# Kernel tuning notes

Measured on AMD Instinct MI355X. Metric: run time of the kernel, lower is better.

The kernel has to match this reference:

```python
import jax, jax.numpy as jnp
import numpy as np

B, K, NQ = 16, 4, 10  # batch, n_blocks, n_qubits
DIM = 2 ** NQ


def setup_inputs() -> dict:
    key = jax.random.key(0)
    k1, k2 = jax.random.split(key)
    weights = jax.random.normal(k1, (B, K, 1, NQ, 1, 1), dtype=jnp.float32)
    state = jax.random.normal(k2, (B, K, 1, DIM, 1), dtype=jnp.float32)
    return {"weights": weights, "state": state}


def _rx_mats(weights):
    # weights: (B, K, 1, NQ, 1, 1) real angles -> per-qubit Rx 2x2: [[cos, -i sin], [-i sin, cos]]
    w = weights[..., 0, 0]  # (B, K, 1, NQ)
    a = jnp.cos(w / 2).astype(jnp.complex64)
    b = jnp.sin(w / 2).astype(jnp.complex64)
    eye = jnp.eye(2, dtype=jnp.complex64)
    offx = jnp.array([[0.0, 1.0], [1.0, 0.0]], dtype=jnp.complex64)
    return a[..., None, None] * eye - 1j * b[..., None, None] * offx  # (B,K,1,NQ,2,2)


def _kron_chain(rxs):
    # rxs: (B, K, 1, NQ, 2, 2) -> U: (B, K, 1, 2**NQ, 2**NQ)
    U = rxs[..., 0, :, :]
    for q in range(1, rxs.shape[-3]):
        m = U.shape[-1]
        Rq = rxs[..., q, :, :]
        # kron(U, Rq): outer product over matrix indices, then merge
        U = (U[..., :, None, :, None] * Rq[..., None, :, None, :]).reshape(*U.shape[:-2], 2 * m, 2 * m)
    return U


def reference(weights, state):
    U = _kron_chain(_rx_mats(weights))              # (B,K,1,2^n,2^n) complex64
    psi = state.astype(jnp.complex64)               # (B,K,1,2^n,1)
    return jnp.matmul(U, psi)                       # (B,K,1,2^n,1) complex64
```

## Files before the change

### kernel.cpp

```cpp
#include <hip/hip_runtime.h>

constexpr int BK  = 16 * 4;
constexpr int NQ  = 10;
constexpr int DIM = 1 << NQ;

__global__ __launch_bounds__(512)
void rx_layer_kernel(const float* __restrict__ weights,
                     const float* __restrict__ state,
                     float* __restrict__ out_re,
                     float* __restrict__ out_im)
{
    __shared__ float re[DIM];
    __shared__ float im[DIM];

    const int bk = blockIdx.x;
    const int t  = threadIdx.x;

    const float* st = state + bk * DIM;
    re[t]       = st[t];       im[t]       = 0.0f;
    re[t + 512] = st[t + 512]; im[t + 512] = 0.0f;

    const float* w = weights + bk * NQ;

    #pragma unroll
    for (int q = 0; q < NQ; ++q) {
        __syncthreads();
        const float wv = w[q];
        const float a  = cosf(0.5f * wv);
        const float b  = sinf(0.5f * wv);

        const int s  = 1 << (NQ - 1 - q);
        const int i0 = ((t & ~(s - 1)) << 1) | (t & (s - 1));
        const int i1 = i0 + s;

        const float x0r = re[i0], x0i = im[i0];
        const float x1r = re[i1], x1i = im[i1];

        re[i0] = a * x0r + b * x1i;
        im[i0] = a * x0i - b * x1r;
        re[i1] = a * x1r + b * x0i;
        im[i1] = a * x1i - b * x0r;
    }
    __syncthreads();

    float* orr = out_re + bk * DIM;
    orr[t]       = re[t];
    orr[t + 512] = re[t + 512];
    if (out_im != nullptr) {
        float* oi = out_im + bk * DIM;
        oi[t]       = im[t];
        oi[t + 512] = im[t + 512];
    }
}

extern "C" void kernel_launch(void* const* d_in, const int* in_sizes, int n_in,
                              void* d_out, int out_size, void* d_ws, size_t ws_size,
                              hipStream_t stream) {
    const float* weights = (const float*)d_in[0];
    const float* state   = (const float*)d_in[1];
    float* out = (float*)d_out;

    float* out_re = out;
    float* out_im = nullptr;
    if (out_size >= 2 * BK * DIM) {
        out_im = out + BK * DIM;
    }
    rx_layer_kernel<<<BK, 512, 0, stream>>>(weights, state, out_re, out_im);
}
```

Baseline: 57.57 us.

## Apply Rx gates in registers with one wavefront per block using lane shuffles

Replaces the 512-thread shared-memory kernel, which needed a barrier per qubit, with a single 64-lane wavefront per state vector that holds 16 amplitudes per lane in registers. High qubits are applied through cross-lane shuffles and low qubits through in-register butterflies. The first gate uses the fact that the input is real to skip the imaginary work. It drops all LDS traffic and __syncthreads, and vectorises global loads and stores with float4. The trade-off is far fewer threads in flight (64 blocks of 64 threads) and an unconditional write of the imaginary output.

Result: no change. 57.89 us (+0.6%).

```diff
diff --git a/kernel.cpp b/kernel.cpp
--- a/kernel.cpp
+++ b/kernel.cpp
@@ -4,52 +4,77 @@
 constexpr int NQ  = 10;
 constexpr int DIM = 1 << NQ;
 
-__global__ __launch_bounds__(512)
+__global__ __launch_bounds__(64)
 void rx_layer_kernel(const float* __restrict__ weights,
                      const float* __restrict__ state,
                      float* __restrict__ out_re,
                      float* __restrict__ out_im)
 {
-    __shared__ float re[DIM];
-    __shared__ float im[DIM];
+    const int bk   = blockIdx.x;
+    const int lane = threadIdx.x;
 
-    const int bk = blockIdx.x;
-    const int t  = threadIdx.x;
+    float xr[16], xi[16];
 
-    const float* st = state + bk * DIM;
-    re[t]       = st[t];       im[t]       = 0.0f;
-    re[t + 512] = st[t + 512]; im[t + 512] = 0.0f;
+    const float4* st = reinterpret_cast<const float4*>(state + bk * DIM) + lane * 4;
+    #pragma unroll
+    for (int j = 0; j < 4; ++j) {
+        float4 v = st[j];
+        xr[4*j+0] = v.x; xr[4*j+1] = v.y; xr[4*j+2] = v.z; xr[4*j+3] = v.w;
+    }
 
     const float* w = weights + bk * NQ;
 
+    {
+        const float wv = w[0];
+        const float a = cosf(0.5f * wv), b = sinf(0.5f * wv);
+        #pragma unroll
+        for (int r = 0; r < 16; ++r) {
+            const float pr = __shfl_xor(xr[r], 32, 64);
+            xi[r] = -b * pr;
+            xr[r] =  a * xr[r];
+        }
+    }
+
     #pragma unroll
-    for (int q = 0; q < NQ; ++q) {
-        __syncthreads();
+    for (int q = 1; q < 6; ++q) {
         const float wv = w[q];
-        const float a  = cosf(0.5f * wv);
-        const float b  = sinf(0.5f * wv);
+        const float a = cosf(0.5f * wv), b = sinf(0.5f * wv);
+        const int mask = 1 << (5 - q);
+        #pragma unroll
+        for (int r = 0; r < 16; ++r) {
+            const float pr = __shfl_xor(xr[r], mask, 64);
+            const float pi = __shfl_xor(xi[r], mask, 64);
+            const float nr = fmaf(a, xr[r],  b * pi);
+            const float ni = fmaf(a, xi[r], -b * pr);
+            xr[r] = nr; xi[r] = ni;
+        }
+    }
 
-        const int s  = 1 << (NQ - 1 - q);
-        const int i0 = ((t & ~(s - 1)) << 1) | (t & (s - 1));
-        const int i1 = i0 + s;
+    #pragma unroll
+    for (int q = 6; q < 10; ++q) {
+        const float wv = w[q];
+        const float a = cosf(0.5f * wv), b = sinf(0.5f * wv);
+        const int s = 1 << (9 - q);
+        #pragma unroll
+        for (int r = 0; r < 16; ++r) {
+            if (!(r & s)) {
+                const int r1 = r | s;
+                const float x0r = xr[r],  x0i = xi[r];
+                const float x1r = xr[r1], x1i = xi[r1];
+                xr[r]  = fmaf(a, x0r,  b * x1i);
+                xi[r]  = fmaf(a, x0i, -b * x1r);
+                xr[r1] = fmaf(a, x1r,  b * x0i);
+                xi[r1] = fmaf(a, x1i, -b * x0r);
+            }
+        }
+    }
 
-        const float x0r = re[i0], x0i = im[i0];
-        const float x1r = re[i1], x1i = im[i1];
-
-        re[i0] = a * x0r + b * x1i;
-        im[i0] = a * x0i - b * x1r;
-        re[i1] = a * x1r + b * x0i;
-        im[i1] = a * x1i - b * x0r;
-    }
-    __syncthreads();
-
-    float* orr = out_re + bk * DIM;
-    orr[t]       = re[t];
-    orr[t + 512] = re[t + 512];
-    if (out_im != nullptr) {
-        float* oi = out_im + bk * DIM;
-        oi[t]       = im[t];
-        oi[t + 512] = im[t + 512];
+    float4* orr = reinterpret_cast<float4*>(out_re + bk * DIM) + lane * 4;
+    float4* oi  = reinterpret_cast<float4*>(out_im + bk * DIM) + lane * 4;
+    #pragma unroll
+    for (int j = 0; j < 4; ++j) {
+        orr[j] = make_float4(xr[4*j+0], xr[4*j+1], xr[4*j+2], xr[4*j+3]);
+        oi[j]  = make_float4(xi[4*j+0], xi[4*j+1], xi[4*j+2], xi[4*j+3]);
     }
 }
 
@@ -60,10 +85,5 @@
     const float* state   = (const float*)d_in[1];
     float* out = (float*)d_out;
 
-    float* out_re = out;
-    float* out_im = nullptr;
-    if (out_size >= 2 * BK * DIM) {
-        out_im = out + BK * DIM;
-    }
-    rx_layer_kernel<<<BK, 512, 0, stream>>>(weights, state, out_re, out_im);
+    rx_layer_kernel<<<BK, 64, 0, stream>>>(weights, state, out, out + BK * DIM);
 }
```
